# Kernel tuning notes

Hardware: AMD Instinct MI355X
Metric: run time of the kernel (lower is better)

## Reference

```python
import jax, jax.numpy as jnp
import numpy as np

N = 100000   # num_nodes
E = 300000   # num_edges
R = 200      # num_rels
B = 32       # num_bases (bdd blocks)
H = 128      # h_dim
SI = H // B  # submat_in = 4


def setup_inputs() -> dict:
    key = jax.random.key(0)
    ks = jax.random.split(key, 10)
    return {
        "node_ids": jnp.arange(N, dtype=jnp.int32),
        "src": jax.random.randint(ks[0], (E,), 0, N, dtype=jnp.int32),
        "dst": jax.random.randint(ks[1], (E,), 0, N, dtype=jnp.int32),
        "etypes": jax.random.randint(ks[2], (E,), 0, R, dtype=jnp.int32),
        "norm": jax.random.uniform(ks[3], (E, 1), dtype=jnp.float32),
        "emb": jax.random.normal(ks[4], (N, H), dtype=jnp.float32) * 0.02,
        "W1": jax.random.normal(ks[5], (R, B, SI, SI), dtype=jnp.float32) / np.float32(np.sqrt(SI)),
        "loop_w1": jax.random.normal(ks[6], (H, H), dtype=jnp.float32) / np.float32(np.sqrt(H)),
        "bias1": jnp.zeros((H,), dtype=jnp.float32),
        "W2": jax.random.normal(ks[7], (R, B, SI, 2 * SI), dtype=jnp.float32) / np.float32(np.sqrt(SI)),
        "loop_w2": jax.random.normal(ks[8], (H, 2 * H), dtype=jnp.float32) / np.float32(np.sqrt(H)),
        "bias2": jnp.zeros((2 * H,), dtype=jnp.float32),
        "eps": jax.random.normal(ks[9], (N, H), dtype=jnp.float32),
    }


def rel_graph_conv_bdd(h, src, dst, etypes, norm, W, loop_w, bias):
    """DGL RelGraphConv with regularizer='bdd', self_loop=True, bias=True."""
    _, Bb, si, so = W.shape
    h_src = h[src].reshape(-1, Bb, si)                  # (E, B, si)
    We = W[etypes]                                      # (E, B, si, so) gathered block weights
    msg = jnp.einsum('ebi,ebio->ebo', h_src, We).reshape(-1, Bb * so)  # (E, out)
    msg = msg * norm                                    # edge norm
    agg = jax.ops.segment_sum(msg, dst, num_segments=N)  # scatter-add to dst
    return agg + bias + h @ loop_w


def reference(node_ids, src, dst, etypes, norm, emb, W1, loop_w1, bias1, W2, loop_w2, bias2, eps):
    h = emb[node_ids]                                   # embedding lookup (N, H)
    h = jax.nn.relu(rel_graph_conv_bdd(h, src, dst, etypes, norm, W1, loop_w1, bias1))
    h = rel_graph_conv_bdd(h, src, dst, etypes, norm, W2, loop_w2, bias2)  # (N, 2H)
    # utils.gaussian_parameters: split last dim, v = softplus + 1e-8
    m, h_pre = jnp.split(h, 2, axis=-1)
    v = jax.nn.softplus(h_pre) + 1e-8
    # utils.sample_gaussian: reparameterized sample
    z = m + jnp.sqrt(v) * eps
    return z
```

## Files before the change

### kernel.cpp

```cpp
#include <hip/hip_runtime.h>
#include <math.h>

#define HD 128

union F4 { float4 v; float f[4]; };

__device__ __forceinline__ float dot4(const F4& a, const F4& b){
  return fmaf(a.f[0], b.f[0], fmaf(a.f[1], b.f[1], fmaf(a.f[2], b.f[2], a.f[3]*b.f[3])));
}

__global__ void k_count(const int* __restrict__ dst, int* __restrict__ counts, int E){
  int e = blockIdx.x*256 + threadIdx.x;
  if (e < E) atomicAdd(&counts[dst[e]], 1);
}

__global__ void k_scan_block(const int* __restrict__ counts, int* __restrict__ scanTmp,
                             int* __restrict__ blockSums, int n){
  __shared__ int sm[256];
  int i = blockIdx.x*256 + threadIdx.x;
  int v = (i<n)?counts[i]:0;
  sm[threadIdx.x]=v; __syncthreads();
  for (int ofs=1; ofs<256; ofs<<=1){
    int t = (threadIdx.x>=ofs)?sm[threadIdx.x-ofs]:0;
    __syncthreads();
    sm[threadIdx.x]+=t;
    __syncthreads();
  }
  if (i<n) scanTmp[i]=sm[threadIdx.x];
  if (threadIdx.x==255) blockSums[blockIdx.x]=sm[255];
}

__global__ void k_scan_top(int* __restrict__ blockSums, int nb){
  __shared__ int sm[1024];
  int v = ((int)threadIdx.x<nb)?blockSums[threadIdx.x]:0;
  sm[threadIdx.x]=v; __syncthreads();
  for (int ofs=1; ofs<1024; ofs<<=1){
    int t = ((int)threadIdx.x>=ofs)?sm[threadIdx.x-ofs]:0;
    __syncthreads();
    sm[threadIdx.x]+=t;
    __syncthreads();
  }
  if ((int)threadIdx.x<nb) blockSums[threadIdx.x] = sm[threadIdx.x]-v;
}

__global__ void k_scan_fin(const int* __restrict__ scanTmp, const int* __restrict__ blockSums,
                           const int* __restrict__ counts,
                           int* __restrict__ row_ptr, int* __restrict__ cursors, int n){
  int i = blockIdx.x*256 + threadIdx.x;
  if (i<n){
    int incl = scanTmp[i] + blockSums[blockIdx.x];
    row_ptr[i+1] = incl;
    cursors[i] = incl - counts[i];
  }
  if (i==0) row_ptr[0]=0;
}

__global__ void k_scatter(const int* __restrict__ dst, const int* __restrict__ src,
                          const int* __restrict__ et, const float* __restrict__ norm,
                          int* __restrict__ cursors, int4* __restrict__ pay, int E){
  int e = blockIdx.x*256 + threadIdx.x;
  if (e<E){
    int p = atomicAdd(&cursors[dst[e]],1);
    pay[p] = make_int4(src[e], et[e], __float_as_int(norm[e]), 0);
  }
}

__global__ void k_w1t(const float* __restrict__ W, float* __restrict__ WT, int n){
  int d = blockIdx.x*256 + threadIdx.x;
  if (d < n){
    int i = d & 3, o = (d>>2) & 3, rb = d>>4;
    WT[d] = W[rb*16 + i*4 + o];
  }
}
__global__ void k_w2t(const float* __restrict__ W, float* __restrict__ WT, int n){
  int d = blockIdx.x*256 + threadIdx.x;
  if (d < n){
    int i = d & 3, o = (d>>2) & 7, rb = d>>5;
    WT[d] = W[rb*32 + i*8 + o];
  }
}

__global__ void k_gather(const int* __restrict__ ids, const float4* __restrict__ emb4,
                         float4* __restrict__ h0, int nf4){
  int i = blockIdx.x*256+threadIdx.x;
  if (i<nf4){
    int row = i>>5, c = i&31;
    h0[i] = emb4[ids[row]*32 + c];
  }
}

__global__ __launch_bounds__(256)
void k_edge1(const int* __restrict__ row_ptr, const int4* __restrict__ pay,
             const float* __restrict__ h, const float* __restrict__ WT,
             float* __restrict__ agg, int Nn){
  int wid = (blockIdx.x*256 + threadIdx.x)>>6;
  wid = __builtin_amdgcn_readfirstlane(wid);
  int lane = threadIdx.x & 63;
  if (wid >= Nn) return;
  int e0 = row_ptr[wid], e1 = row_ptr[wid+1];
  int b0 = lane>>2, o = lane&3;
  float acc0=0.f, acc1=0.f;
  for (int e=e0; e<e1; e+=2){
    int4 p0 = pay[e];
    bool has2 = (e+1 < e1);
    int4 p1 = has2 ? pay[e+1] : p0;
    float n0 = __int_as_float(p0.z);
    float n1 = has2 ? __int_as_float(p1.z) : 0.f;
    const float* ha = &h[p0.x*HD];  const float* wa = &WT[p0.y*512];
    const float* hb = &h[p1.x*HD];  const float* wb = &WT[p1.y*512];
    F4 hA0,hB0,wA0,wB0,hA1,hB1,wA1,wB1;
    hA0.v = *(const float4*)&ha[b0*4];
    hB0.v = *(const float4*)&ha[(b0+16)*4];
    wA0.v = *(const float4*)&wa[b0*16 + o*4];
    wB0.v = *(const float4*)&wa[(b0+16)*16 + o*4];
    hA1.v = *(const float4*)&hb[b0*4];
    hB1.v = *(const float4*)&hb[(b0+16)*4];
    wA1.v = *(const float4*)&wb[b0*16 + o*4];
    wB1.v = *(const float4*)&wb[(b0+16)*16 + o*4];
    acc0 = fmaf(n0, dot4(hA0,wA0), acc0);
    acc1 = fmaf(n0, dot4(hB0,wB0), acc1);
    acc0 = fmaf(n1, dot4(hA1,wA1), acc0);
    acc1 = fmaf(n1, dot4(hB1,wB1), acc1);
  }
  agg[wid*HD + lane]      = acc0;
  agg[wid*HD + 64 + lane] = acc1;
}

__global__ __launch_bounds__(256)
void k_edge2(const int* __restrict__ row_ptr, const int4* __restrict__ pay,
             const float* __restrict__ h, const float* __restrict__ WT,
             float* __restrict__ agg, int Nn){
  int wid = (blockIdx.x*256 + threadIdx.x)>>6;
  wid = __builtin_amdgcn_readfirstlane(wid);
  int lane = threadIdx.x & 63;
  if (wid >= Nn) return;
  int e0 = row_ptr[wid], e1 = row_ptr[wid+1];
  int ob = lane>>3, o = lane&7;
  float acc[4] = {0.f,0.f,0.f,0.f};
  for (int e=e0; e<e1; e+=2){
    int4 p0 = pay[e];
    bool has2 = (e+1 < e1);
    int4 p1 = has2 ? pay[e+1] : p0;
    float n0 = __int_as_float(p0.z);
    float n1 = has2 ? __int_as_float(p1.z) : 0.f;
    const float* ha = &h[p0.x*HD];  const float* wa = &WT[p0.y*1024];
    const float* hb = &h[p1.x*HD];  const float* wb = &WT[p1.y*1024];
    F4 hva[4], wva[4], hvb[4], wvb[4];
    #pragma unroll
    for (int u=0; u<4; ++u){
      int b = ob + 8*u;
      hva[u].v = *(const float4*)&ha[b*4];
      wva[u].v = *(const float4*)&wa[b*32 + o*4];
      hvb[u].v = *(const float4*)&hb[b*4];
      wvb[u].v = *(const float4*)&wb[b*32 + o*4];
    }
    #pragma unroll
    for (int u=0; u<4; ++u){
      acc[u] = fmaf(n0, dot4(hva[u],wva[u]), acc[u]);
      acc[u] = fmaf(n1, dot4(hvb[u],wvb[u]), acc[u]);
    }
  }
  #pragma unroll
  for (int u=0; u<4; ++u) agg[wid*256 + u*64 + lane] = acc[u];
}

template<int EPI>
__device__ __forceinline__ void gemm_body(const float* __restrict__ A,
                  const float* __restrict__ W,
                  const float* __restrict__ agg, const float* __restrict__ bias,
                  const float* __restrict__ eps, float* __restrict__ out,
                  int M, int rowBase, int bx){
  constexpr int NO = (EPI==1) ? 128 : 256;
  __shared__ __align__(16) float As[32*132];
  __shared__ __align__(16) float Bs[32*132];
  const int tid = threadIdx.x;
  const int cg = tid & 15, rg = tid >> 4;
  float acc[8][2][4];
  #pragma unroll
  for (int i=0;i<8;++i)
    #pragma unroll
    for (int g=0;g<2;++g)
      #pragma unroll
      for (int j=0;j<4;++j) acc[i][g][j]=0.f;

  for (int kt=0; kt<4; ++kt){
    #pragma unroll
    for (int it=0; it<4; ++it){
      int idx = it*256 + tid;
      int ar = idx>>3, ac4 = idx&7;
      int gr = rowBase + ar;
      F4 v; v.v = make_float4(0.f,0.f,0.f,0.f);
      if (gr < M) v.v = *(const float4*)&A[gr*HD + kt*32 + ac4*4];
      #pragma unroll
      for (int j=0;j<4;++j) As[(ac4*4+j)*132 + ar] = v.f[j];
    }
    #pragma unroll
    for (int it=0; it<4; ++it){
      int idx = it*256 + tid;
      int wr = idx>>5, wc4 = idx&31;
      int gcol = (EPI==1) ? wc4*4
               : ((wc4<16) ? bx*64 + wc4*4 : 128 + bx*64 + (wc4-16)*4);
      *(float4*)&Bs[wr*132 + wc4*4] = *(const float4*)&W[(kt*32+wr)*NO + gcol];
    }
    __syncthreads();
    #pragma unroll 8
    for (int kk=0; kk<32; ++kk){
      F4 a0, a1, b0, b1;
      a0.v = *(const float4*)&As[kk*132 + rg*8];
      a1.v = *(const float4*)&As[kk*132 + rg*8 + 4];
      b0.v = *(const float4*)&Bs[kk*132 + cg*4];
      b1.v = *(const float4*)&Bs[kk*132 + cg*4 + 64];
      #pragma unroll
      for (int i=0;i<4;++i)
        #pragma unroll
        for (int j=0;j<4;++j){
          acc[i][0][j]   = fmaf(a0.f[i], b0.f[j], acc[i][0][j]);
          acc[i][1][j]   = fmaf(a0.f[i], b1.f[j], acc[i][1][j]);
          acc[i+4][0][j] = fmaf(a1.f[i], b0.f[j], acc[i+4][0][j]);
          acc[i+4][1][j] = fmaf(a1.f[i], b1.f[j], acc[i+4][1][j]);
        }
    }
    __syncthreads();
  }

  #pragma unroll
  for (int i=0;i<8;++i){
    int r = rowBase + rg*8 + i;
    if (r >= M) continue;
    if (EPI==1){
      #pragma unroll
      for (int g=0;g<2;++g){
        int col0 = cg*4 + 64*g;
        F4 ag; ag.v = *(const float4*)&agg[r*128 + col0];
        F4 bs; bs.v = *(const float4*)&bias[col0];
        F4 o;
        #pragma unroll
        for (int j=0;j<4;++j) o.f[j] = fmaxf(acc[i][g][j] + ag.f[j] + bs.f[j], 0.f);
        *(float4*)&out[r*128 + col0] = o.v;
      }
    } else {
      int colm = bx*64 + cg*4;
      F4 agm;  agm.v  = *(const float4*)&agg[r*256 + colm];
      F4 aghp; aghp.v = *(const float4*)&agg[r*256 + colm + 128];
      F4 bsm;  bsm.v  = *(const float4*)&bias[colm];
      F4 bshp; bshp.v = *(const float4*)&bias[colm + 128];
      F4 ep;   ep.v   = *(const float4*)&eps[r*128 + colm];
      F4 z;
      #pragma unroll
      for (int j=0;j<4;++j){
        float m  = acc[i][0][j] + agm.f[j]  + bsm.f[j];
        float hp = acc[i][1][j] + aghp.f[j] + bshp.f[j];
        float sp = fmaxf(hp, 0.f) + log1pf(expf(-fabsf(hp)));
        z.f[j] = fmaf(sqrtf(sp + 1e-8f), ep.f[j], m);
      }
      *(float4*)&out[r*128 + colm] = z.v;
    }
  }
}

__global__ __launch_bounds__(256, 4)
void k_gemm_relu(const float* __restrict__ A, const float* __restrict__ W,
                 const float* __restrict__ agg, const float* __restrict__ bias,
                 float* __restrict__ out, int M){
  gemm_body<1>(A, W, agg, bias, nullptr, out, M, blockIdx.x*128, 0);
}

__global__ __launch_bounds__(256, 4)
void k_gemm_gauss(const float* __restrict__ A, const float* __restrict__ W,
                  const float* __restrict__ agg, const float* __restrict__ bias,
                  const float* __restrict__ eps, float* __restrict__ out, int M){
  gemm_body<2>(A, W, agg, bias, eps, out, M, (blockIdx.x>>1)*128, blockIdx.x&1);
}

extern "C" void kernel_launch(void* const* d_in, const int* in_sizes, int n_in,
                              void* d_out, int out_size, void* d_ws, size_t ws_size,
                              hipStream_t stream){
  (void)n_in; (void)out_size; (void)ws_size;
  const int*   node_ids = (const int*)d_in[0];
  const int*   src  = (const int*)d_in[1];
  const int*   dst  = (const int*)d_in[2];
  const int*   et   = (const int*)d_in[3];
  const float* norm = (const float*)d_in[4];
  const float* emb  = (const float*)d_in[5];
  const float* W1   = (const float*)d_in[6];
  const float* lw1  = (const float*)d_in[7];
  const float* b1   = (const float*)d_in[8];
  const float* W2   = (const float*)d_in[9];
  const float* lw2  = (const float*)d_in[10];
  const float* b2   = (const float*)d_in[11];
  const float* eps  = (const float*)d_in[12];
  float* out = (float*)d_out;

  const int N  = in_sizes[0];
  const int E  = in_sizes[1];
  const int n1 = in_sizes[6];
  const int n2 = in_sizes[9];

  char* w = (char*)d_ws;
  size_t szNH = (size_t)N*HD*sizeof(float);
  float* h0   = (float*)(w);
  float* agg2 = (float*)(w);
  float* h1   = (float*)(w + 2*szNH);
  float* agg1 = (float*)(w + 3*szNH);
  char*  ip   = w + 4*szNH;
  int4*  pay       = (int4*)ip;
  int*   counts    = (int*)(pay + E);
  int*   scanTmp   = counts + N;
  int*   row_ptr   = scanTmp + N;
  int*   cursors   = row_ptr + (N+1);
  int*   blockSums = cursors + N;
  float* W1T       = (float*)(blockSums + 1024);
  float* W2T       = W1T + n1;

  hipMemsetAsync(counts, 0, (size_t)N*sizeof(int), stream);

  int nb_e    = (E+255)/256;
  int nb_scan = (N+255)/256;

  k_w1t<<<(n1+255)/256, 256, 0, stream>>>(W1, W1T, n1);
  k_w2t<<<(n2+255)/256, 256, 0, stream>>>(W2, W2T, n2);
  k_gather<<<(N*32+255)/256, 256, 0, stream>>>(node_ids, (const float4*)emb, (float4*)h0, N*32);
  k_count<<<nb_e, 256, 0, stream>>>(dst, counts, E);
  k_scan_block<<<nb_scan, 256, 0, stream>>>(counts, scanTmp, blockSums, N);
  k_scan_top<<<1, 1024, 0, stream>>>(blockSums, nb_scan);
  k_scan_fin<<<nb_scan, 256, 0, stream>>>(scanTmp, blockSums, counts, row_ptr, cursors, N);
  k_scatter<<<nb_e, 256, 0, stream>>>(dst, src, et, norm, cursors, pay, E);

  int nb_rows = (N+3)/4;
  int nb_g    = (N+127)/128;

  k_edge1<<<nb_rows, 256, 0, stream>>>(row_ptr, pay, h0, W1T, agg1, N);
  k_gemm_relu<<<nb_g, 256, 0, stream>>>(h0, lw1, agg1, b1, h1, N);
  k_edge2<<<nb_rows, 256, 0, stream>>>(row_ptr, pay, h1, W2T, agg2, N);
  k_gemm_gauss<<<nb_g*2, 256, 0, stream>>>(h1, lw2, agg2, b2, eps, out, N);
}
```

Before: 518.7 us.

## Replace FP32 self-loop GEMMs with bf16 MFMA kernels and packed weights

Replaces the shared-memory FP32 SIMT GEMMs for the self-loop matmuls with bf16 MFMA 16x16x32 kernels. Weights are pre-packed into MFMA fragment order, and activations get extra bf16 copies written by the gather and relu epilogue. This is meant to cut the FP32 FMA cost of the N×128×128 and N×128×256 matmuls, at the cost of lower precision, additional bf16 activation writes, and uncoalesced scalar epilogue stores. Accuracy drops to bf16 inputs with fp32 accumulation.

Result: faster. 430.5 us (-17.0%).

```diff
diff --git a/kernel.cpp b/kernel.cpp
--- a/kernel.cpp
+++ b/kernel.cpp
@@ -5,8 +5,16 @@
 
 union F4 { float4 v; float f[4]; };
 
+typedef __attribute__((ext_vector_type(8))) short bf8_t;
+typedef __attribute__((ext_vector_type(4))) float f4_t;
+
 __device__ __forceinline__ float dot4(const F4& a, const F4& b){
   return fmaf(a.f[0], b.f[0], fmaf(a.f[1], b.f[1], fmaf(a.f[2], b.f[2], a.f[3]*b.f[3])));
+}
+
+__device__ __forceinline__ unsigned short f2bf(float f){
+  unsigned int u = __float_as_uint(f);
+  return (unsigned short)((u + 0x7fffu + ((u>>16)&1u)) >> 16);
 }
 
 __global__ void k_count(const int* __restrict__ dst, int* __restrict__ counts, int E){
@@ -80,12 +88,28 @@
   }
 }
 
+__global__ void k_wpack(const float* __restrict__ W, unsigned short* __restrict__ Wp,
+                        int NCT, int NO){
+  int t = blockIdx.x*256 + threadIdx.x;
+  if (t >= NCT*256) return;
+  int lane = t & 63, ks = (t>>6) & 3, ct = t >> 8;
+  int k0 = ks*32 + (lane>>4)*8, col = ct*16 + (lane&15);
+  unsigned short v[8];
+  #pragma unroll
+  for (int j=0;j<8;++j) v[j] = f2bf(W[(k0+j)*NO + col]);
+  ushort4* dst = (ushort4*)&Wp[(size_t)t*8];
+  dst[0] = make_ushort4(v[0],v[1],v[2],v[3]);
+  dst[1] = make_ushort4(v[4],v[5],v[6],v[7]);
+}
+
 __global__ void k_gather(const int* __restrict__ ids, const float4* __restrict__ emb4,
-                         float4* __restrict__ h0, int nf4){
+                         float4* __restrict__ h0, unsigned short* __restrict__ h0b, int nf4){
   int i = blockIdx.x*256+threadIdx.x;
   if (i<nf4){
     int row = i>>5, c = i&31;
-    h0[i] = emb4[ids[row]*32 + c];
+    float4 v = emb4[ids[row]*32 + c];
+    h0[i] = v;
+    *(ushort4*)&h0b[(size_t)i*4] = make_ushort4(f2bf(v.x),f2bf(v.y),f2bf(v.z),f2bf(v.w));
   }
 }
 
@@ -164,112 +188,79 @@
   for (int u=0; u<4; ++u) agg[wid*256 + u*64 + lane] = acc[u];
 }
 
-template<int EPI>
-__device__ __forceinline__ void gemm_body(const float* __restrict__ A,
-                  const float* __restrict__ W,
-                  const float* __restrict__ agg, const float* __restrict__ bias,
-                  const float* __restrict__ eps, float* __restrict__ out,
-                  int M, int rowBase, int bx){
-  constexpr int NO = (EPI==1) ? 128 : 256;
-  __shared__ __align__(16) float As[32*132];
-  __shared__ __align__(16) float Bs[32*132];
-  const int tid = threadIdx.x;
-  const int cg = tid & 15, rg = tid >> 4;
-  float acc[8][2][4];
-  #pragma unroll
-  for (int i=0;i<8;++i)
-    #pragma unroll
-    for (int g=0;g<2;++g)
-      #pragma unroll
-      for (int j=0;j<4;++j) acc[i][g][j]=0.f;
-
-  for (int kt=0; kt<4; ++kt){
-    #pragma unroll
-    for (int it=0; it<4; ++it){
-      int idx = it*256 + tid;
-      int ar = idx>>3, ac4 = idx&7;
-      int gr = rowBase + ar;
-      F4 v; v.v = make_float4(0.f,0.f,0.f,0.f);
-      if (gr < M) v.v = *(const float4*)&A[gr*HD + kt*32 + ac4*4];
-      #pragma unroll
-      for (int j=0;j<4;++j) As[(ac4*4+j)*132 + ar] = v.f[j];
-    }
-    #pragma unroll
-    for (int it=0; it<4; ++it){
-      int idx = it*256 + tid;
-      int wr = idx>>5, wc4 = idx&31;
-      int gcol = (EPI==1) ? wc4*4
-               : ((wc4<16) ? bx*64 + wc4*4 : 128 + bx*64 + (wc4-16)*4);
-      *(float4*)&Bs[wr*132 + wc4*4] = *(const float4*)&W[(kt*32+wr)*NO + gcol];
-    }
-    __syncthreads();
-    #pragma unroll 8
-    for (int kk=0; kk<32; ++kk){
-      F4 a0, a1, b0, b1;
-      a0.v = *(const float4*)&As[kk*132 + rg*8];
-      a1.v = *(const float4*)&As[kk*132 + rg*8 + 4];
-      b0.v = *(const float4*)&Bs[kk*132 + cg*4];
-      b1.v = *(const float4*)&Bs[kk*132 + cg*4 + 64];
-      #pragma unroll
-      for (int i=0;i<4;++i)
-        #pragma unroll
-        for (int j=0;j<4;++j){
-          acc[i][0][j]   = fmaf(a0.f[i], b0.f[j], acc[i][0][j]);
-          acc[i][1][j]   = fmaf(a0.f[i], b1.f[j], acc[i][1][j]);
-          acc[i+4][0][j] = fmaf(a1.f[i], b0.f[j], acc[i+4][0][j]);
-          acc[i+4][1][j] = fmaf(a1.f[i], b1.f[j], acc[i+4][1][j]);
-        }
-    }
-    __syncthreads();
-  }
-
-  #pragma unroll
-  for (int i=0;i<8;++i){
-    int r = rowBase + rg*8 + i;
-    if (r >= M) continue;
-    if (EPI==1){
-      #pragma unroll
-      for (int g=0;g<2;++g){
-        int col0 = cg*4 + 64*g;
-        F4 ag; ag.v = *(const float4*)&agg[r*128 + col0];
-        F4 bs; bs.v = *(const float4*)&bias[col0];
-        F4 o;
-        #pragma unroll
-        for (int j=0;j<4;++j) o.f[j] = fmaxf(acc[i][g][j] + ag.f[j] + bs.f[j], 0.f);
-        *(float4*)&out[r*128 + col0] = o.v;
-      }
-    } else {
-      int colm = bx*64 + cg*4;
-      F4 agm;  agm.v  = *(const float4*)&agg[r*256 + colm];
-      F4 aghp; aghp.v = *(const float4*)&agg[r*256 + colm + 128];
-      F4 bsm;  bsm.v  = *(const float4*)&bias[colm];
-      F4 bshp; bshp.v = *(const float4*)&bias[colm + 128];
-      F4 ep;   ep.v   = *(const float4*)&eps[r*128 + colm];
-      F4 z;
-      #pragma unroll
-      for (int j=0;j<4;++j){
-        float m  = acc[i][0][j] + agm.f[j]  + bsm.f[j];
-        float hp = acc[i][1][j] + aghp.f[j] + bshp.f[j];
-        float sp = fmaxf(hp, 0.f) + log1pf(expf(-fabsf(hp)));
-        z.f[j] = fmaf(sqrtf(sp + 1e-8f), ep.f[j], m);
-      }
-      *(float4*)&out[r*128 + colm] = z.v;
-    }
-  }
-}
-
-__global__ __launch_bounds__(256, 4)
-void k_gemm_relu(const float* __restrict__ A, const float* __restrict__ W,
+__global__ __launch_bounds__(256)
+void k_mfma_relu(const unsigned short* __restrict__ Ab, const unsigned short* __restrict__ Wp,
                  const float* __restrict__ agg, const float* __restrict__ bias,
-                 float* __restrict__ out, int M){
-  gemm_body<1>(A, W, agg, bias, nullptr, out, M, blockIdx.x*128, 0);
-}
-
-__global__ __launch_bounds__(256, 4)
-void k_gemm_gauss(const float* __restrict__ A, const float* __restrict__ W,
+                 float* __restrict__ out, unsigned short* __restrict__ outb, int M){
+  const int lane = threadIdx.x & 63;
+  const int rowBase = blockIdx.x*64 + (threadIdx.x>>6)*16;
+  const int ar = lane & 15, kg = lane >> 4;
+  const int aclamp = min(rowBase + ar, M-1);
+  f4_t acc[8];
+  #pragma unroll
+  for (int ct=0; ct<8; ++ct) acc[ct] = (f4_t)0.f;
+  #pragma unroll
+  for (int ks=0; ks<4; ++ks){
+    bf8_t a = *(const bf8_t*)&Ab[(size_t)aclamp*HD + ks*32 + kg*8];
+    #pragma unroll
+    for (int ct=0; ct<8; ++ct){
+      bf8_t b = *(const bf8_t*)&Wp[(size_t)((ct*4 + ks)*64 + lane)*8];
+      acc[ct] = __builtin_amdgcn_mfma_f32_16x16x32_bf16(a, b, acc[ct], 0,0,0);
+    }
+  }
+  const int crow = rowBase + kg*4;
+  #pragma unroll
+  for (int r=0; r<4; ++r){
+    int gr = crow + r;
+    if (gr >= M) continue;
+    #pragma unroll
+    for (int ct=0; ct<8; ++ct){
+      int col = ct*16 + ar;
+      float v = fmaxf(acc[ct][r] + agg[(size_t)gr*128 + col] + bias[col], 0.f);
+      out[(size_t)gr*128 + col] = v;
+      outb[(size_t)gr*128 + col] = f2bf(v);
+    }
+  }
+}
+
+__global__ __launch_bounds__(256)
+void k_mfma_gauss(const unsigned short* __restrict__ Ab, const unsigned short* __restrict__ Wp,
                   const float* __restrict__ agg, const float* __restrict__ bias,
                   const float* __restrict__ eps, float* __restrict__ out, int M){
-  gemm_body<2>(A, W, agg, bias, eps, out, M, (blockIdx.x>>1)*128, blockIdx.x&1);
+  const int lane = threadIdx.x & 63;
+  const int bx = blockIdx.x & 1;
+  const int rowBase = (blockIdx.x>>1)*64 + (threadIdx.x>>6)*16;
+  const int ar = lane & 15, kg = lane >> 4;
+  const int aclamp = min(rowBase + ar, M-1);
+  f4_t accm[4], acch[4];
+  #pragma unroll
+  for (int ct=0; ct<4; ++ct){ accm[ct] = (f4_t)0.f; acch[ct] = (f4_t)0.f; }
+  #pragma unroll
+  for (int ks=0; ks<4; ++ks){
+    bf8_t a = *(const bf8_t*)&Ab[(size_t)aclamp*HD + ks*32 + kg*8];
+    #pragma unroll
+    for (int ct=0; ct<4; ++ct){
+      int ctm = bx*4 + ct, cth = 8 + bx*4 + ct;
+      bf8_t bm = *(const bf8_t*)&Wp[(size_t)((ctm*4 + ks)*64 + lane)*8];
+      bf8_t bh = *(const bf8_t*)&Wp[(size_t)((cth*4 + ks)*64 + lane)*8];
+      accm[ct] = __builtin_amdgcn_mfma_f32_16x16x32_bf16(a, bm, accm[ct], 0,0,0);
+      acch[ct] = __builtin_amdgcn_mfma_f32_16x16x32_bf16(a, bh, acch[ct], 0,0,0);
+    }
+  }
+  const int crow = rowBase + kg*4;
+  #pragma unroll
+  for (int r=0; r<4; ++r){
+    int gr = crow + r;
+    if (gr >= M) continue;
+    #pragma unroll
+    for (int ct=0; ct<4; ++ct){
+      int colm = bx*64 + ct*16 + ar;
+      float m  = accm[ct][r] + agg[(size_t)gr*256 + colm]       + bias[colm];
+      float hp = acch[ct][r] + agg[(size_t)gr*256 + colm + 128] + bias[colm+128];
+      float sp = fmaxf(hp, 0.f) + log1pf(expf(-fabsf(hp)));
+      out[(size_t)gr*128 + colm] = fmaf(sqrtf(sp + 1e-8f), eps[(size_t)gr*128 + colm], m);
+    }
+  }
 }
 
 extern "C" void kernel_launch(void* const* d_in, const int* in_sizes, int n_in,
@@ -311,6 +302,11 @@
   int*   blockSums = cursors + N;
   float* W1T       = (float*)(blockSums + 1024);
   float* W2T       = W1T + n1;
+  size_t tail      = ((size_t)((char*)(W2T + n2) - w) + 63) & ~(size_t)63;
+  unsigned short* W1p = (unsigned short*)(w + tail);
+  unsigned short* W2p = W1p + 8*256*8;
+  unsigned short* h0b = W2p + 16*256*8;
+  unsigned short* h1b = h0b + (size_t)N*HD;
 
   hipMemsetAsync(counts, 0, (size_t)N*sizeof(int), stream);
 
@@ -319,7 +315,9 @@
 
   k_w1t<<<(n1+255)/256, 256, 0, stream>>>(W1, W1T, n1);
   k_w2t<<<(n2+255)/256, 256, 0, stream>>>(W2, W2T, n2);
-  k_gather<<<(N*32+255)/256, 256, 0, stream>>>(node_ids, (const float4*)emb, (float4*)h0, N*32);
+  k_wpack<<<8, 256, 0, stream>>>(lw1, W1p, 8, 128);
+  k_wpack<<<16, 256, 0, stream>>>(lw2, W2p, 16, 256);
+  k_gather<<<(N*32+255)/256, 256, 0, stream>>>(node_ids, (const float4*)emb, (float4*)h0, h0b, N*32);
   k_count<<<nb_e, 256, 0, stream>>>(dst, counts, E);
   k_scan_block<<<nb_scan, 256, 0, stream>>>(counts, scanTmp, blockSums, N);
   k_scan_top<<<1, 1024, 0, stream>>>(blockSums, nb_scan);
@@ -327,10 +325,10 @@
   k_scatter<<<nb_e, 256, 0, stream>>>(dst, src, et, norm, cursors, pay, E);
 
   int nb_rows = (N+3)/4;
-  int nb_g    = (N+127)/128;
+  int nb_m    = (N+63)/64;
 
   k_edge1<<<nb_rows, 256, 0, stream>>>(row_ptr, pay, h0, W1T, agg1, N);
-  k_gemm_relu<<<nb_g, 256, 0, stream>>>(h0, lw1, agg1, b1, h1, N);
+  k_mfma_relu<<<nb_m, 256, 0, stream>>>(h0b, W1p, agg1, b1, h1, h1b, N);
   k_edge2<<<nb_rows, 256, 0, stream>>>(row_ptr, pay, h1, W2T, agg2, N);
-  k_gemm_gauss<<<nb_g*2, 256, 0, stream>>>(h1, lw2, agg2, b2, eps, out, N);
-}
+  k_mfma_gauss<<<nb_m*2, 256, 0, stream>>>(h1b, W2p, agg2, b2, eps, out, N);
+}
```
